# Kernel optimization log

Hardware: AMD Instinct MI355X
Metric: run time of the kernel (lower is better)

## Reference

```python
import jax, jax.numpy as jnp
import numpy as np

E = 8      # num_expert
D = 1024   # d_model
H = 2048   # expert hidden (htoh4 size)
K = 2      # top_k
N = 2048   # tokens (batch*seq)


def setup_inputs() -> dict:
    key = jax.random.key(0)
    ks = jax.random.split(key, 4)
    sc = lambda k, shape, s: jax.random.normal(k, shape, jnp.float32) * s
    return {
        "inp": jax.random.normal(ks[0], (N, D), jnp.float32),
        "Wg": sc(ks[1], (D, E), D ** -0.5),          # NaiveGate linear
        "bg": jnp.zeros((E,), jnp.float32),
        "W1": sc(ks[2], (E, D, H), D ** -0.5),        # per-expert htoh4
        "b1": jnp.zeros((E, H), jnp.float32),
        "W2": sc(ks[3], (E, H, D), H ** -0.5),        # per-expert h4toh
        "b2": jnp.zeros((E, D), jnp.float32),
    }


def reference(inp, Wg, bg, W1, b1, W2, b2):
    # NaiveGate: linear -> top_k logits -> softmax over the k selected logits
    logits = inp @ Wg + bg                              # [N, E]
    top_val, top_idx = jax.lax.top_k(logits, K)         # [N, K]
    gate_score = jax.nn.softmax(top_val, axis=-1)       # [N, K]

    # Expert grouped compute. Reference computes every expert on every token
    # (exact math, no capacity dropping); combine selects the routed ones.
    h = jax.nn.gelu(jnp.einsum('nd,edh->neh', inp, W1) + b1)   # [N, E, H]
    y = jnp.einsum('neh,ehd->ned', h, W2) + b2                 # [N, E, D]

    # Combine: equivalent to bmm(gate_score[N,1,K], x[N,K,D]) after gather.
    comb = jnp.sum(jax.nn.one_hot(top_idx, E, dtype=inp.dtype)
                   * gate_score[..., None], axis=1)            # [N, E]
    return jnp.einsum('ne,ned->nd', comb, y)                   # [N, D]
```

## Files before the change

kernel.cpp:

```cpp
#include <hip/hip_runtime.h>
#include <math.h>

#define N_TOK 2048
#define DM    1024
#define HD    2048
#define NE    8
#define RMAX  5120
#define TMAX  40

#define GATE_BLKS 512
#define XCVT_BLKS 1024
#define PREP_BLKS (GATE_BLKS + XCVT_BLKS)

typedef short short8 __attribute__((ext_vector_type(8)));
typedef unsigned short u16x8 __attribute__((ext_vector_type(8)));
typedef float f32x4  __attribute__((ext_vector_type(4)));

__device__ inline unsigned short f2b(float f) {
  unsigned int u = __float_as_uint(f);
  return (unsigned short)((u + 0x7FFFu + ((u >> 16) & 1u)) >> 16);
}
__device__ inline float b2f(unsigned short s) {
  return __uint_as_float(((unsigned int)s) << 16);
}
__device__ inline void gload_lds16(const void* g, void* l) {
  __builtin_amdgcn_global_load_lds(
      (const __attribute__((address_space(1))) unsigned int*)g,
      (__attribute__((address_space(3))) unsigned int*)l, 16, 0, 0);
}

__global__ __launch_bounds__(256) void prep_kernel(
    const float* __restrict__ inp, const float* __restrict__ Wg,
    const float* __restrict__ bg,
    int* __restrict__ top_idx, float* __restrict__ gate_w,
    unsigned short* __restrict__ Xb) {
  int bid = blockIdx.x;
  if (bid < GATE_BLKS) {
    int wave = threadIdx.x >> 6;
    int lane = threadIdx.x & 63;
    int n = bid * 4 + wave;
    float acc[NE];
#pragma unroll
    for (int e = 0; e < NE; ++e) acc[e] = 0.f;
    const float4* wg4 = reinterpret_cast<const float4*>(Wg);
#pragma unroll
    for (int i = 0; i < DM / 64; ++i) {
      int d = i * 64 + lane;
      float x = inp[n * DM + d];
      float4 w0 = wg4[d * 2 + 0];
      float4 w1 = wg4[d * 2 + 1];
      acc[0] += x * w0.x; acc[1] += x * w0.y; acc[2] += x * w0.z; acc[3] += x * w0.w;
      acc[4] += x * w1.x; acc[5] += x * w1.y; acc[6] += x * w1.z; acc[7] += x * w1.w;
    }
#pragma unroll
    for (int off = 32; off > 0; off >>= 1) {
#pragma unroll
      for (int e = 0; e < NE; ++e) acc[e] += __shfl_xor(acc[e], off);
    }
    if (lane == 0) {
      float v0 = -1e30f, v1 = -1e30f; int i0 = -1, i1 = -1;
#pragma unroll
      for (int e = 0; e < NE; ++e) {
        float v = acc[e] + bg[e];
        if (v > v0)      { v1 = v0; i1 = i0; v0 = v; i0 = e; }
        else if (v > v1) { v1 = v;  i1 = e; }
      }
      float e1 = expf(v1 - v0);
      float s  = 1.f + e1;
      top_idx[n * 2]     = i0;
      top_idx[n * 2 + 1] = i1;
      gate_w[n * 2]      = 1.f / s;
      gate_w[n * 2 + 1]  = e1 / s;
    }
  } else {
    int i = ((bid - GATE_BLKS) * 256 + threadIdx.x) * 8;
    float4 a = *(const float4*)(inp + i);
    float4 b = *(const float4*)(inp + i + 4);
    ushort4 pa, pb;
    pa.x = f2b(a.x); pa.y = f2b(a.y); pa.z = f2b(a.z); pa.w = f2b(a.w);
    pb.x = f2b(b.x); pb.y = f2b(b.y); pb.z = f2b(b.z); pb.w = f2b(b.w);
    *(ushort4*)(Xb + i)     = pa;
    *(ushort4*)(Xb + i + 4) = pb;
  }
}

__global__ __launch_bounds__(1024) void group_kernel(
    const int* __restrict__ top_idx,
    int* __restrict__ token_of, int* __restrict__ inv_g,
    int* __restrict__ tile_expert, int* __restrict__ tile_row0,
    int* __restrict__ n_tiles) {
  __shared__ int s_wtot[16];
  int tid = threadIdx.x, lane = tid & 63, wid = tid >> 6;
  int base = 0, tiles = 0;
  for (int e = 0; e < NE; ++e) {
    int cnt = 0;
#pragma unroll
    for (int c0 = 0; c0 < N_TOK; c0 += 1024) {
      int n = c0 + tid;
      int t0 = top_idx[n * 2], t1 = top_idx[n * 2 + 1];
      bool f = (t0 == e) || (t1 == e);
      int k = (t0 == e) ? 0 : 1;
      unsigned long long m = __ballot(f);
      int lp = __popcll(m & ((1ull << lane) - 1ull));
      if (lane == 0) s_wtot[wid] = __popcll(m);
      __syncthreads();
      int wbase = 0, tot = 0;
#pragma unroll
      for (int w = 0; w < 16; ++w) {
        int c = s_wtot[w];
        if (w < wid) wbase += c;
        tot += c;
      }
      if (f) {
        int pos = base + cnt + wbase + lp;
        token_of[pos] = n;
        inv_g[n * 2 + k] = pos;
      }
      cnt += tot;
      __syncthreads();
    }
    int padded = (cnt + 127) & ~127;
    for (int i = cnt + tid; i < padded; i += 1024) token_of[base + i] = -1;
    if (tid == 0) {
      for (int t = 0; t < padded / 128; ++t) {
        tile_expert[tiles + t] = e;
        tile_row0[tiles + t]   = base + t * 128;
      }
    }
    tiles += padded / 128;
    base  += padded;
    __syncthreads();
  }
  if (tid == 0) n_tiles[0] = tiles;
}

__global__ __launch_bounds__(256) void ffn1_mfma(
    const unsigned short* __restrict__ Xb,
    const float* __restrict__ W1,
    const float* __restrict__ b1,
    const unsigned short* __restrict__ zbuf,
    const int* __restrict__ token_of, const int* __restrict__ tile_expert,
    const int* __restrict__ tile_row0, const int* __restrict__ n_tiles,
    unsigned short* __restrict__ Hbuf) {
  if ((int)blockIdx.x >= n_tiles[0]) return;
  int e    = tile_expert[blockIdx.x];
  int row0 = tile_row0[blockIdx.x];
  int h0   = blockIdx.y * 64;
  __shared__ __align__(16) unsigned short Asl[128][32];
  __shared__ __align__(16) unsigned short Bsl[4][64][8];
  int tid = threadIdx.x, lane = tid & 63;
  int wid = tid >> 6, wr = wid >> 1, wc = wid & 1;
  int l15 = lane & 15, l4 = lane >> 4;
  int sw  = (l15 >> 1) & 3;

  int ar[2], asg[2], tk[2];
#pragma unroll
  for (int q = 0; q < 2; ++q) {
    int idx = tid + q * 256;
    ar[q]  = idx >> 2;
    asg[q] = (idx & 3) ^ ((ar[q] >> 1) & 3);
    tk[q]  = token_of[row0 + ar[q]];
  }
  int bcol = tid & 63, bks = tid >> 6;
  const float* bsrc = W1 + (size_t)e * DM * HD + (size_t)(bks * 8) * HD + h0 + bcol;

  f32x4 acc[4][2] = {};

  for (int kc = 0; kc < DM; kc += 32) {
    __syncthreads();
    float bv[8];
#pragma unroll
    for (int i = 0; i < 8; ++i) bv[i] = bsrc[(size_t)i * HD];
    bsrc += (size_t)32 * HD;
#pragma unroll
    for (int q = 0; q < 2; ++q) {
      int idx = tid + q * 256;
      const unsigned short* ga = (tk[q] < 0)
          ? zbuf
          : Xb + (size_t)tk[q] * DM + kc + asg[q] * 8;
      gload_lds16(ga, (char*)&Asl[0][0] + (size_t)idx * 16);
    }
    u16x8 bo;
#pragma unroll
    for (int i = 0; i < 8; ++i) bo[i] = f2b(bv[i]);
    *(u16x8*)&Bsl[bks][bcol][0] = bo;
    __syncthreads();
    short8 a[4], b[2];
#pragma unroll
    for (int m = 0; m < 4; ++m) {
      int R = wr * 64 + m * 16 + l15;
      a[m] = *(const short8*)((const char*)&Asl[0][0] + R * 64 + ((l4 ^ sw) << 4));
    }
#pragma unroll
    for (int n = 0; n < 2; ++n)
      b[n] = *(const short8*)&Bsl[l4][wc * 32 + n * 16 + l15][0];
#pragma unroll
    for (int m = 0; m < 4; ++m)
#pragma unroll
      for (int n = 0; n < 2; ++n)
        acc[m][n] = __builtin_amdgcn_mfma_f32_16x16x32_bf16(a[m], b[n], acc[m][n], 0, 0, 0);
  }

  float bias[2];
#pragma unroll
  for (int n = 0; n < 2; ++n) bias[n] = b1[e * HD + h0 + wc * 32 + n * 16 + l15];
#pragma unroll
  for (int m = 0; m < 4; ++m) {
#pragma unroll
    for (int n = 0; n < 2; ++n) {
      int col = h0 + wc * 32 + n * 16 + l15;
#pragma unroll
      for (int j = 0; j < 4; ++j) {
        int row = row0 + wr * 64 + m * 16 + l4 * 4 + j;
        float x = acc[m][n][j] + bias[n];
        float g = 0.5f * x * (1.f + tanhf(0.7978845608f * (x + 0.044715f * x * x * x)));
        Hbuf[(size_t)row * HD + col] = f2b(g);
      }
    }
  }
}

__global__ __launch_bounds__(256) void ffn2_mfma(
    const unsigned short* __restrict__ Hbuf,
    const float* __restrict__ W2,
    const float* __restrict__ b2,
    const int* __restrict__ tile_expert, const int* __restrict__ tile_row0,
    const int* __restrict__ n_tiles,
    unsigned short* __restrict__ Ybuf) {
  if ((int)blockIdx.x >= n_tiles[0]) return;
  int e    = tile_expert[blockIdx.x];
  int row0 = tile_row0[blockIdx.x];
  int d0   = blockIdx.y * 64;
  __shared__ __align__(16) unsigned short Asl[128][32];
  __shared__ __align__(16) unsigned short Bsl[4][64][8];
  int tid = threadIdx.x, lane = tid & 63;
  int wid = tid >> 6, wr = wid >> 1, wc = wid & 1;
  int l15 = lane & 15, l4 = lane >> 4;
  int sw  = (l15 >> 1) & 3;

  int ar[2], asg[2];
#pragma unroll
  for (int q = 0; q < 2; ++q) {
    int idx = tid + q * 256;
    ar[q]  = idx >> 2;
    asg[q] = (idx & 3) ^ ((ar[q] >> 1) & 3);
  }
  int bcol = tid & 63, bks = tid >> 6;
  const float* bsrc = W2 + (size_t)e * HD * DM + (size_t)(bks * 8) * DM + d0 + bcol;

  f32x4 acc[4][2] = {};

  for (int kc = 0; kc < HD; kc += 32) {
    __syncthreads();
    float bv[8];
#pragma unroll
    for (int i = 0; i < 8; ++i) bv[i] = bsrc[(size_t)i * DM];
    bsrc += (size_t)32 * DM;
#pragma unroll
    for (int q = 0; q < 2; ++q) {
      int idx = tid + q * 256;
      const unsigned short* ga =
          Hbuf + (size_t)(row0 + ar[q]) * HD + kc + asg[q] * 8;
      gload_lds16(ga, (char*)&Asl[0][0] + (size_t)idx * 16);
    }
    u16x8 bo;
#pragma unroll
    for (int i = 0; i < 8; ++i) bo[i] = f2b(bv[i]);
    *(u16x8*)&Bsl[bks][bcol][0] = bo;
    __syncthreads();
    short8 a[4], b[2];
#pragma unroll
    for (int m = 0; m < 4; ++m) {
      int R = wr * 64 + m * 16 + l15;
      a[m] = *(const short8*)((const char*)&Asl[0][0] + R * 64 + ((l4 ^ sw) << 4));
    }
#pragma unroll
    for (int n = 0; n < 2; ++n)
      b[n] = *(const short8*)&Bsl[l4][wc * 32 + n * 16 + l15][0];
#pragma unroll
    for (int m = 0; m < 4; ++m)
#pragma unroll
      for (int n = 0; n < 2; ++n)
        acc[m][n] = __builtin_amdgcn_mfma_f32_16x16x32_bf16(a[m], b[n], acc[m][n], 0, 0, 0);
  }

  float bias[2];
#pragma unroll
  for (int n = 0; n < 2; ++n) bias[n] = b2[e * DM + d0 + wc * 32 + n * 16 + l15];
#pragma unroll
  for (int m = 0; m < 4; ++m) {
#pragma unroll
    for (int n = 0; n < 2; ++n) {
      int col = d0 + wc * 32 + n * 16 + l15;
#pragma unroll
      for (int j = 0; j < 4; ++j) {
        int row = row0 + wr * 64 + m * 16 + l4 * 4 + j;
        Ybuf[(size_t)row * DM + col] = f2b(acc[m][n][j] + bias[n]);
      }
    }
  }
}

__global__ void combine_kernel(const unsigned short* __restrict__ Ybuf,
                               const int* __restrict__ inv_g,
                               const float* __restrict__ gate_w,
                               float* __restrict__ out) {
  int n = blockIdx.x;
  int r0 = inv_g[n * 2], r1 = inv_g[n * 2 + 1];
  float g0 = gate_w[n * 2], g1 = gate_w[n * 2 + 1];
  int i = threadIdx.x;
  ushort4 a = *(const ushort4*)(Ybuf + (size_t)r0 * DM + i * 4);
  ushort4 b = *(const ushort4*)(Ybuf + (size_t)r1 * DM + i * 4);
  float4 rv;
  rv.x = g0 * b2f(a.x) + g1 * b2f(b.x);
  rv.y = g0 * b2f(a.y) + g1 * b2f(b.y);
  rv.z = g0 * b2f(a.z) + g1 * b2f(b.z);
  rv.w = g0 * b2f(a.w) + g1 * b2f(b.w);
  *(float4*)(out + (size_t)n * DM + i * 4) = rv;
}

extern "C" void kernel_launch(void* const* d_in, const int* in_sizes, int n_in,
                              void* d_out, int out_size, void* d_ws, size_t ws_size,
                              hipStream_t stream) {
  const float* inp = (const float*)d_in[0];
  const float* Wg  = (const float*)d_in[1];
  const float* bg  = (const float*)d_in[2];
  const float* W1  = (const float*)d_in[3];
  const float* b1  = (const float*)d_in[4];
  const float* W2  = (const float*)d_in[5];
  const float* b2  = (const float*)d_in[6];
  float* out = (float*)d_out;

  char* ws = (char*)d_ws;
  size_t off = 0;
  auto alloc = [&](size_t bytes) {
    size_t o = off;
    off = (off + bytes + 255) & ~(size_t)255;
    return o;
  };
  int*   top_idx     = (int*)  (ws + alloc(N_TOK * 2 * sizeof(int)));
  float* gate_w      = (float*)(ws + alloc(N_TOK * 2 * sizeof(float)));
  int*   token_of    = (int*)  (ws + alloc(RMAX * sizeof(int)));
  int*   inv_g       = (int*)  (ws + alloc(N_TOK * 2 * sizeof(int)));
  int*   tile_expert = (int*)  (ws + alloc(TMAX * sizeof(int)));
  int*   tile_row0   = (int*)  (ws + alloc(TMAX * sizeof(int)));
  int*   n_tiles     = (int*)  (ws + alloc(sizeof(int)));
  unsigned short* zbuf = (unsigned short*)(ws + alloc(256));
  unsigned short* Xb   = (unsigned short*)(ws + alloc((size_t)N_TOK * DM * 2));
  unsigned short* Hbuf = (unsigned short*)(ws + alloc((size_t)RMAX * HD * 2));
  unsigned short* Ybuf = (unsigned short*)(ws + alloc((size_t)RMAX * DM * 2));
  (void)ws_size;

  hipMemsetAsync(zbuf, 0, 256, stream);
  prep_kernel<<<PREP_BLKS, 256, 0, stream>>>(inp, Wg, bg, top_idx, gate_w, Xb);
  group_kernel<<<1, 1024, 0, stream>>>(top_idx, token_of, inv_g,
                                       tile_expert, tile_row0, n_tiles);
  ffn1_mfma<<<dim3(TMAX, HD / 64), 256, 0, stream>>>(
      Xb, W1, b1, zbuf, token_of, tile_expert, tile_row0, n_tiles, Hbuf);
  ffn2_mfma<<<dim3(TMAX, DM / 64), 256, 0, stream>>>(
      Hbuf, W2, b2, tile_expert, tile_row0, n_tiles, Ybuf);
  combine_kernel<<<N_TOK, 256, 0, stream>>>(Ybuf, inv_g, gate_w, out);
}
```

Measured before the change: 168.0 us.

## Keep per-expert weight slice resident in LDS and loop over row tiles

FFN kernels now launch one block per (expert, output column slice). Each block converts its whole fp32 weight slice to bf16 once into LDS (128 KB), then loops over all 128-row tiles of that expert. A operands are read straight from global memory without LDS staging. This removes the repeated fp32 weight loads and bf16 conversions that previously happened once per row tile. In exchange the grids shrink to 256 blocks, and per-block work scales with expert load, which risks imbalance and low occupancy.

```diff
diff --git a/kernel.cpp b/kernel.cpp
--- a/kernel.cpp
+++ b/kernel.cpp
@@ -6,7 +6,6 @@
 #define HD    2048
 #define NE    8
 #define RMAX  5120
-#define TMAX  40
 
 #define GATE_BLKS 512
 #define XCVT_BLKS 1024
@@ -22,11 +21,6 @@
 }
 __device__ inline float b2f(unsigned short s) {
   return __uint_as_float(((unsigned int)s) << 16);
-}
-__device__ inline void gload_lds16(const void* g, void* l) {
-  __builtin_amdgcn_global_load_lds(
-      (const __attribute__((address_space(1))) unsigned int*)g,
-      (__attribute__((address_space(3))) unsigned int*)l, 16, 0, 0);
 }
 
 __global__ __launch_bounds__(256) void prep_kernel(
@@ -87,11 +81,10 @@
 __global__ __launch_bounds__(1024) void group_kernel(
     const int* __restrict__ top_idx,
     int* __restrict__ token_of, int* __restrict__ inv_g,
-    int* __restrict__ tile_expert, int* __restrict__ tile_row0,
-    int* __restrict__ n_tiles) {
+    int* __restrict__ exp_base, int* __restrict__ exp_nt) {
   __shared__ int s_wtot[16];
   int tid = threadIdx.x, lane = tid & 63, wid = tid >> 6;
-  int base = 0, tiles = 0;
+  int base = 0;
   for (int e = 0; e < NE; ++e) {
     int cnt = 0;
 #pragma unroll
@@ -121,181 +114,144 @@
     }
     int padded = (cnt + 127) & ~127;
     for (int i = cnt + tid; i < padded; i += 1024) token_of[base + i] = -1;
-    if (tid == 0) {
-      for (int t = 0; t < padded / 128; ++t) {
-        tile_expert[tiles + t] = e;
-        tile_row0[tiles + t]   = base + t * 128;
-      }
-    }
-    tiles += padded / 128;
-    base  += padded;
+    if (tid == 0) { exp_base[e] = base; exp_nt[e] = padded / 128; }
+    base += padded;
     __syncthreads();
   }
-  if (tid == 0) n_tiles[0] = tiles;
-}
-
-__global__ __launch_bounds__(256) void ffn1_mfma(
+}
+
+__global__ __launch_bounds__(512, 2) void ffn1_mfma(
     const unsigned short* __restrict__ Xb,
     const float* __restrict__ W1,
     const float* __restrict__ b1,
-    const unsigned short* __restrict__ zbuf,
-    const int* __restrict__ token_of, const int* __restrict__ tile_expert,
-    const int* __restrict__ tile_row0, const int* __restrict__ n_tiles,
+    const unsigned short* __restrict__ Xzero,
+    const int* __restrict__ token_of,
+    const int* __restrict__ exp_base, const int* __restrict__ exp_nt,
     unsigned short* __restrict__ Hbuf) {
-  if ((int)blockIdx.x >= n_tiles[0]) return;
-  int e    = tile_expert[blockIdx.x];
-  int row0 = tile_row0[blockIdx.x];
-  int h0   = blockIdx.y * 64;
-  __shared__ __align__(16) unsigned short Asl[128][32];
-  __shared__ __align__(16) unsigned short Bsl[4][64][8];
+  int e  = blockIdx.x;
+  int h0 = blockIdx.y * 64;
+  __shared__ __align__(16) unsigned short Wl[128][64][8];
   int tid = threadIdx.x, lane = tid & 63;
   int wid = tid >> 6, wr = wid >> 1, wc = wid & 1;
   int l15 = lane & 15, l4 = lane >> 4;
-  int sw  = (l15 >> 1) & 3;
-
-  int ar[2], asg[2], tk[2];
-#pragma unroll
-  for (int q = 0; q < 2; ++q) {
-    int idx = tid + q * 256;
-    ar[q]  = idx >> 2;
-    asg[q] = (idx & 3) ^ ((ar[q] >> 1) & 3);
-    tk[q]  = token_of[row0 + ar[q]];
-  }
-  int bcol = tid & 63, bks = tid >> 6;
-  const float* bsrc = W1 + (size_t)e * DM * HD + (size_t)(bks * 8) * HD + h0 + bcol;
-
-  f32x4 acc[4][2] = {};
-
-  for (int kc = 0; kc < DM; kc += 32) {
-    __syncthreads();
-    float bv[8];
-#pragma unroll
-    for (int i = 0; i < 8; ++i) bv[i] = bsrc[(size_t)i * HD];
-    bsrc += (size_t)32 * HD;
-#pragma unroll
-    for (int q = 0; q < 2; ++q) {
-      int idx = tid + q * 256;
-      const unsigned short* ga = (tk[q] < 0)
-          ? zbuf
-          : Xb + (size_t)tk[q] * DM + kc + asg[q] * 8;
-      gload_lds16(ga, (char*)&Asl[0][0] + (size_t)idx * 16);
-    }
-    u16x8 bo;
-#pragma unroll
-    for (int i = 0; i < 8; ++i) bo[i] = f2b(bv[i]);
-    *(u16x8*)&Bsl[bks][bcol][0] = bo;
-    __syncthreads();
-    short8 a[4], b[2];
-#pragma unroll
-    for (int m = 0; m < 4; ++m) {
-      int R = wr * 64 + m * 16 + l15;
-      a[m] = *(const short8*)((const char*)&Asl[0][0] + R * 64 + ((l4 ^ sw) << 4));
-    }
-#pragma unroll
-    for (int n = 0; n < 2; ++n)
-      b[n] = *(const short8*)&Bsl[l4][wc * 32 + n * 16 + l15][0];
-#pragma unroll
-    for (int m = 0; m < 4; ++m)
-#pragma unroll
-      for (int n = 0; n < 2; ++n)
-        acc[m][n] = __builtin_amdgcn_mfma_f32_16x16x32_bf16(a[m], b[n], acc[m][n], 0, 0, 0);
-  }
+
+  {
+    const float* W1e = W1 + (size_t)e * DM * HD + h0;
+    int scol = tid & 63, skg = tid >> 6;
+#pragma unroll
+    for (int kko = 0; kko < 16; ++kko) {
+      int kb = kko * 8 + skg;
+      const float* s = W1e + (size_t)(kb * 8) * HD + scol;
+      float v[8];
+#pragma unroll
+      for (int i = 0; i < 8; ++i) v[i] = s[(size_t)i * HD];
+      u16x8 o;
+#pragma unroll
+      for (int i = 0; i < 8; ++i) o[i] = f2b(v[i]);
+      *(u16x8*)&Wl[kb][scol][0] = o;
+    }
+  }
+  __syncthreads();
 
   float bias[2];
 #pragma unroll
   for (int n = 0; n < 2; ++n) bias[n] = b1[e * HD + h0 + wc * 32 + n * 16 + l15];
-#pragma unroll
-  for (int m = 0; m < 4; ++m) {
-#pragma unroll
-    for (int n = 0; n < 2; ++n) {
-      int col = h0 + wc * 32 + n * 16 + l15;
-#pragma unroll
-      for (int j = 0; j < 4; ++j) {
-        int row = row0 + wr * 64 + m * 16 + l4 * 4 + j;
-        float x = acc[m][n][j] + bias[n];
-        float g = 0.5f * x * (1.f + tanhf(0.7978845608f * (x + 0.044715f * x * x * x)));
-        Hbuf[(size_t)row * HD + col] = f2b(g);
-      }
-    }
-  }
-}
-
-__global__ __launch_bounds__(256) void ffn2_mfma(
+
+  int nt = exp_nt[e];
+  int base0 = exp_base[e];
+  for (int rt = 0; rt < nt; ++rt) {
+    int row0 = base0 + rt * 128;
+    const unsigned short* abase0;
+    const unsigned short* abase1;
+    {
+      int tk0 = token_of[row0 + wr * 32 + l15];
+      int tk1 = token_of[row0 + wr * 32 + 16 + l15];
+      abase0 = (tk0 < 0) ? Xzero : Xb + (size_t)tk0 * DM;
+      abase1 = (tk1 < 0) ? Xzero : Xb + (size_t)tk1 * DM;
+    }
+    f32x4 acc[2][2] = {};
+    for (int ks = 0; ks < 32; ++ks) {
+      short8 a0 = *(const short8*)(abase0 + ks * 32 + l4 * 8);
+      short8 a1 = *(const short8*)(abase1 + ks * 32 + l4 * 8);
+      short8 b0 = *(const short8*)&Wl[ks * 4 + l4][wc * 32 + l15][0];
+      short8 b1v = *(const short8*)&Wl[ks * 4 + l4][wc * 32 + 16 + l15][0];
+      acc[0][0] = __builtin_amdgcn_mfma_f32_16x16x32_bf16(a0, b0,  acc[0][0], 0, 0, 0);
+      acc[0][1] = __builtin_amdgcn_mfma_f32_16x16x32_bf16(a0, b1v, acc[0][1], 0, 0, 0);
+      acc[1][0] = __builtin_amdgcn_mfma_f32_16x16x32_bf16(a1, b0,  acc[1][0], 0, 0, 0);
+      acc[1][1] = __builtin_amdgcn_mfma_f32_16x16x32_bf16(a1, b1v, acc[1][1], 0, 0, 0);
+    }
+#pragma unroll
+    for (int m = 0; m < 2; ++m) {
+#pragma unroll
+      for (int n = 0; n < 2; ++n) {
+        int col = h0 + wc * 32 + n * 16 + l15;
+#pragma unroll
+        for (int j = 0; j < 4; ++j) {
+          int row = row0 + wr * 32 + m * 16 + l4 * 4 + j;
+          float x = acc[m][n][j] + bias[n];
+          float g = 0.5f * x * (1.f + tanhf(0.7978845608f * (x + 0.044715f * x * x * x)));
+          Hbuf[(size_t)row * HD + col] = f2b(g);
+        }
+      }
+    }
+  }
+}
+
+__global__ __launch_bounds__(512, 2) void ffn2_mfma(
     const unsigned short* __restrict__ Hbuf,
     const float* __restrict__ W2,
     const float* __restrict__ b2,
-    const int* __restrict__ tile_expert, const int* __restrict__ tile_row0,
-    const int* __restrict__ n_tiles,
+    const int* __restrict__ exp_base, const int* __restrict__ exp_nt,
     unsigned short* __restrict__ Ybuf) {
-  if ((int)blockIdx.x >= n_tiles[0]) return;
-  int e    = tile_expert[blockIdx.x];
-  int row0 = tile_row0[blockIdx.x];
-  int d0   = blockIdx.y * 64;
-  __shared__ __align__(16) unsigned short Asl[128][32];
-  __shared__ __align__(16) unsigned short Bsl[4][64][8];
+  int e  = blockIdx.x;
+  int d0 = blockIdx.y * 32;
+  __shared__ __align__(16) unsigned short Wl[256][32][8];
   int tid = threadIdx.x, lane = tid & 63;
-  int wid = tid >> 6, wr = wid >> 1, wc = wid & 1;
+  int wr = tid >> 6;
   int l15 = lane & 15, l4 = lane >> 4;
-  int sw  = (l15 >> 1) & 3;
-
-  int ar[2], asg[2];
-#pragma unroll
-  for (int q = 0; q < 2; ++q) {
-    int idx = tid + q * 256;
-    ar[q]  = idx >> 2;
-    asg[q] = (idx & 3) ^ ((ar[q] >> 1) & 3);
-  }
-  int bcol = tid & 63, bks = tid >> 6;
-  const float* bsrc = W2 + (size_t)e * HD * DM + (size_t)(bks * 8) * DM + d0 + bcol;
-
-  f32x4 acc[4][2] = {};
-
-  for (int kc = 0; kc < HD; kc += 32) {
-    __syncthreads();
-    float bv[8];
-#pragma unroll
-    for (int i = 0; i < 8; ++i) bv[i] = bsrc[(size_t)i * DM];
-    bsrc += (size_t)32 * DM;
-#pragma unroll
-    for (int q = 0; q < 2; ++q) {
-      int idx = tid + q * 256;
-      const unsigned short* ga =
-          Hbuf + (size_t)(row0 + ar[q]) * HD + kc + asg[q] * 8;
-      gload_lds16(ga, (char*)&Asl[0][0] + (size_t)idx * 16);
-    }
-    u16x8 bo;
-#pragma unroll
-    for (int i = 0; i < 8; ++i) bo[i] = f2b(bv[i]);
-    *(u16x8*)&Bsl[bks][bcol][0] = bo;
-    __syncthreads();
-    short8 a[4], b[2];
-#pragma unroll
-    for (int m = 0; m < 4; ++m) {
-      int R = wr * 64 + m * 16 + l15;
-      a[m] = *(const short8*)((const char*)&Asl[0][0] + R * 64 + ((l4 ^ sw) << 4));
-    }
-#pragma unroll
-    for (int n = 0; n < 2; ++n)
-      b[n] = *(const short8*)&Bsl[l4][wc * 32 + n * 16 + l15][0];
-#pragma unroll
-    for (int m = 0; m < 4; ++m)
-#pragma unroll
-      for (int n = 0; n < 2; ++n)
-        acc[m][n] = __builtin_amdgcn_mfma_f32_16x16x32_bf16(a[m], b[n], acc[m][n], 0, 0, 0);
-  }
+
+  {
+    const float* W2e = W2 + (size_t)e * HD * DM + d0;
+    int scol = tid & 31, skg = tid >> 5;
+#pragma unroll
+    for (int kko = 0; kko < 16; ++kko) {
+      int kb = kko * 16 + skg;
+      const float* s = W2e + (size_t)(kb * 8) * DM + scol;
+      float v[8];
+#pragma unroll
+      for (int i = 0; i < 8; ++i) v[i] = s[(size_t)i * DM];
+      u16x8 o;
+#pragma unroll
+      for (int i = 0; i < 8; ++i) o[i] = f2b(v[i]);
+      *(u16x8*)&Wl[kb][scol][0] = o;
+    }
+  }
+  __syncthreads();
 
   float bias[2];
 #pragma unroll
-  for (int n = 0; n < 2; ++n) bias[n] = b2[e * DM + d0 + wc * 32 + n * 16 + l15];
-#pragma unroll
-  for (int m = 0; m < 4; ++m) {
+  for (int n = 0; n < 2; ++n) bias[n] = b2[e * DM + d0 + n * 16 + l15];
+
+  int nt = exp_nt[e];
+  int base0 = exp_base[e];
+  for (int rt = 0; rt < nt; ++rt) {
+    int row0 = base0 + rt * 128;
+    const unsigned short* abase = Hbuf + (size_t)(row0 + wr * 16 + l15) * HD;
+    f32x4 acc[2] = {};
+    for (int ks = 0; ks < 64; ++ks) {
+      short8 a  = *(const short8*)(abase + ks * 32 + l4 * 8);
+      short8 b0 = *(const short8*)&Wl[ks * 4 + l4][l15][0];
+      short8 b1v = *(const short8*)&Wl[ks * 4 + l4][16 + l15][0];
+      acc[0] = __builtin_amdgcn_mfma_f32_16x16x32_bf16(a, b0,  acc[0], 0, 0, 0);
+      acc[1] = __builtin_amdgcn_mfma_f32_16x16x32_bf16(a, b1v, acc[1], 0, 0, 0);
+    }
 #pragma unroll
     for (int n = 0; n < 2; ++n) {
-      int col = d0 + wc * 32 + n * 16 + l15;
+      int col = d0 + n * 16 + l15;
 #pragma unroll
       for (int j = 0; j < 4; ++j) {
-        int row = row0 + wr * 64 + m * 16 + l4 * 4 + j;
-        Ybuf[(size_t)row * DM + col] = f2b(acc[m][n][j] + bias[n]);
+        int row = row0 + wr * 16 + l4 * 4 + j;
+        Ybuf[(size_t)row * DM + col] = f2b(acc[n][j] + bias[n]);
       }
     }
   }
@@ -338,26 +294,24 @@
     off = (off + bytes + 255) & ~(size_t)255;
     return o;
   };
-  int*   top_idx     = (int*)  (ws + alloc(N_TOK * 2 * sizeof(int)));
-  float* gate_w      = (float*)(ws + alloc(N_TOK * 2 * sizeof(float)));
-  int*   token_of    = (int*)  (ws + alloc(RMAX * sizeof(int)));
-  int*   inv_g       = (int*)  (ws + alloc(N_TOK * 2 * sizeof(int)));
-  int*   tile_expert = (int*)  (ws + alloc(TMAX * sizeof(int)));
-  int*   tile_row0   = (int*)  (ws + alloc(TMAX * sizeof(int)));
-  int*   n_tiles     = (int*)  (ws + alloc(sizeof(int)));
-  unsigned short* zbuf = (unsigned short*)(ws + alloc(256));
-  unsigned short* Xb   = (unsigned short*)(ws + alloc((size_t)N_TOK * DM * 2));
-  unsigned short* Hbuf = (unsigned short*)(ws + alloc((size_t)RMAX * HD * 2));
-  unsigned short* Ybuf = (unsigned short*)(ws + alloc((size_t)RMAX * DM * 2));
+  int*   top_idx  = (int*)  (ws + alloc(N_TOK * 2 * sizeof(int)));
+  float* gate_w   = (float*)(ws + alloc(N_TOK * 2 * sizeof(float)));
+  int*   token_of = (int*)  (ws + alloc(RMAX * sizeof(int)));
+  int*   inv_g    = (int*)  (ws + alloc(N_TOK * 2 * sizeof(int)));
+  int*   exp_base = (int*)  (ws + alloc(NE * sizeof(int)));
+  int*   exp_nt   = (int*)  (ws + alloc(NE * sizeof(int)));
+  unsigned short* Xzero = (unsigned short*)(ws + alloc(DM * 2));
+  unsigned short* Xb    = (unsigned short*)(ws + alloc((size_t)N_TOK * DM * 2));
+  unsigned short* Hbuf  = (unsigned short*)(ws + alloc((size_t)RMAX * HD * 2));
+  unsigned short* Ybuf  = (unsigned short*)(ws + alloc((size_t)RMAX * DM * 2));
   (void)ws_size;
 
-  hipMemsetAsync(zbuf, 0, 256, stream);
+  hipMemsetAsync(Xzero, 0, DM * 2, stream);
   prep_kernel<<<PREP_BLKS, 256, 0, stream>>>(inp, Wg, bg, top_idx, gate_w, Xb);
-  group_kernel<<<1, 1024, 0, stream>>>(top_idx, token_of, inv_g,
-                                       tile_expert, tile_row0, n_tiles);
-  ffn1_mfma<<<dim3(TMAX, HD / 64), 256, 0, stream>>>(
-      Xb, W1, b1, zbuf, token_of, tile_expert, tile_row0, n_tiles, Hbuf);
-  ffn2_mfma<<<dim3(TMAX, DM / 64), 256, 0, stream>>>(
-      Hbuf, W2, b2, tile_expert, tile_row0, n_tiles, Ybuf);
+  group_kernel<<<1, 1024, 0, stream>>>(top_idx, token_of, inv_g, exp_base, exp_nt);
+  ffn1_mfma<<<dim3(NE, HD / 64), 512, 0, stream>>>(
+      Xb, W1, b1, Xzero, token_of, exp_base, exp_nt, Hbuf);
+  ffn2_mfma<<<dim3(NE, DM / 32), 512, 0, stream>>>(
+      Hbuf, W2, b2, exp_base, exp_nt, Ybuf);
   combine_kernel<<<N_TOK, 256, 0, stream>>>(Ybuf, inv_g, gate_w, out);
 }
```

Result: slower. 359.4 us (+114.0%).

## Double-buffer LDS tiles in expert FFN GEMMs to overlap loads with MFMA

Applied to the files above, without the earlier changes.

Both expert GEMM kernels now keep two LDS buffers for the A and B tiles. The global loads for the next k-step are issued before the MFMAs of the current step, which removes one barrier per iteration and hides load latency behind compute. Launch bounds now request 4 blocks per CU, which caps register use. The cost is twice the LDS footprint, extra register pressure from holding two B prefetch arrays, and a larger zero buffer for padded rows.

```diff
diff --git a/kernel.cpp b/kernel.cpp
--- a/kernel.cpp
+++ b/kernel.cpp
@@ -134,11 +134,11 @@
   if (tid == 0) n_tiles[0] = tiles;
 }
 
-__global__ __launch_bounds__(256) void ffn1_mfma(
+__global__ __launch_bounds__(256, 4) void ffn1_mfma(
     const unsigned short* __restrict__ Xb,
     const float* __restrict__ W1,
     const float* __restrict__ b1,
-    const unsigned short* __restrict__ zbuf,
+    const unsigned short* __restrict__ Xzero,
     const int* __restrict__ token_of, const int* __restrict__ tile_expert,
     const int* __restrict__ tile_row0, const int* __restrict__ n_tiles,
     unsigned short* __restrict__ Hbuf) {
@@ -146,8 +146,8 @@
   int e    = tile_expert[blockIdx.x];
   int row0 = tile_row0[blockIdx.x];
   int h0   = blockIdx.y * 64;
-  __shared__ __align__(16) unsigned short Asl[128][32];
-  __shared__ __align__(16) unsigned short Bsl[4][64][8];
+  __shared__ __align__(16) unsigned short Asl[2][128][32];
+  __shared__ __align__(16) unsigned short Bsl[2][4][64][8];
   int tid = threadIdx.x, lane = tid & 63;
   int wid = tid >> 6, wr = wid >> 1, wc = wid & 1;
   int l15 = lane & 15, l4 = lane >> 4;
@@ -162,43 +162,60 @@
     tk[q]  = token_of[row0 + ar[q]];
   }
   int bcol = tid & 63, bks = tid >> 6;
-  const float* bsrc = W1 + (size_t)e * DM * HD + (size_t)(bks * 8) * HD + h0 + bcol;
+  const float* W1e = W1 + (size_t)e * DM * HD;
 
   f32x4 acc[4][2] = {};
-
-  for (int kc = 0; kc < DM; kc += 32) {
-    __syncthreads();
-    float bv[8];
-#pragma unroll
-    for (int i = 0; i < 8; ++i) bv[i] = bsrc[(size_t)i * HD];
-    bsrc += (size_t)32 * HD;
+  float bvA[8], bvB[8];
+
+  auto issueB = [&](int t, float* bv) {
+    const float* p = W1e + (size_t)(t * 32 + bks * 8) * HD + h0 + bcol;
+#pragma unroll
+    for (int i = 0; i < 8; ++i) bv[i] = p[(size_t)i * HD];
+  };
+  auto packwrite = [&](const float* bv, int buf) {
+    u16x8 o;
+#pragma unroll
+    for (int i = 0; i < 8; ++i) o[i] = f2b(bv[i]);
+    *(u16x8*)&Bsl[buf][bks][bcol][0] = o;
+  };
+  auto issueA = [&](int t, int buf) {
 #pragma unroll
     for (int q = 0; q < 2; ++q) {
       int idx = tid + q * 256;
       const unsigned short* ga = (tk[q] < 0)
-          ? zbuf
-          : Xb + (size_t)tk[q] * DM + kc + asg[q] * 8;
-      gload_lds16(ga, (char*)&Asl[0][0] + (size_t)idx * 16);
-    }
-    u16x8 bo;
-#pragma unroll
-    for (int i = 0; i < 8; ++i) bo[i] = f2b(bv[i]);
-    *(u16x8*)&Bsl[bks][bcol][0] = bo;
-    __syncthreads();
+          ? Xzero
+          : Xb + (size_t)tk[q] * DM + t * 32 + asg[q] * 8;
+      gload_lds16(ga, (char*)&Asl[buf][0][0] + (size_t)idx * 16);
+    }
+  };
+  auto compute = [&](int buf) {
     short8 a[4], b[2];
 #pragma unroll
     for (int m = 0; m < 4; ++m) {
       int R = wr * 64 + m * 16 + l15;
-      a[m] = *(const short8*)((const char*)&Asl[0][0] + R * 64 + ((l4 ^ sw) << 4));
+      a[m] = *(const short8*)((const char*)&Asl[buf][0][0] + R * 64 + ((l4 ^ sw) << 4));
     }
 #pragma unroll
     for (int n = 0; n < 2; ++n)
-      b[n] = *(const short8*)&Bsl[l4][wc * 32 + n * 16 + l15][0];
+      b[n] = *(const short8*)&Bsl[buf][l4][wc * 32 + n * 16 + l15][0];
 #pragma unroll
     for (int m = 0; m < 4; ++m)
 #pragma unroll
       for (int n = 0; n < 2; ++n)
         acc[m][n] = __builtin_amdgcn_mfma_f32_16x16x32_bf16(a[m], b[n], acc[m][n], 0, 0, 0);
+  };
+
+  issueB(0, bvA);
+  issueA(0, 0);
+  for (int t = 0; t < 32; t += 2) {
+    packwrite(bvA, 0);
+    __syncthreads();
+    if (t + 1 < 32) { issueB(t + 1, bvB); issueA(t + 1, 1); }
+    compute(0);
+    packwrite(bvB, 1);
+    __syncthreads();
+    if (t + 2 < 32) { issueB(t + 2, bvA); issueA(t + 2, 0); }
+    compute(1);
   }
 
   float bias[2];
@@ -220,7 +237,7 @@
   }
 }
 
-__global__ __launch_bounds__(256) void ffn2_mfma(
+__global__ __launch_bounds__(256, 4) void ffn2_mfma(
     const unsigned short* __restrict__ Hbuf,
     const float* __restrict__ W2,
     const float* __restrict__ b2,
@@ -231,8 +248,8 @@
   int e    = tile_expert[blockIdx.x];
   int row0 = tile_row0[blockIdx.x];
   int d0   = blockIdx.y * 64;
-  __shared__ __align__(16) unsigned short Asl[128][32];
-  __shared__ __align__(16) unsigned short Bsl[4][64][8];
+  __shared__ __align__(16) unsigned short Asl[2][128][32];
+  __shared__ __align__(16) unsigned short Bsl[2][4][64][8];
   int tid = threadIdx.x, lane = tid & 63;
   int wid = tid >> 6, wr = wid >> 1, wc = wid & 1;
   int l15 = lane & 15, l4 = lane >> 4;
@@ -246,42 +263,59 @@
     asg[q] = (idx & 3) ^ ((ar[q] >> 1) & 3);
   }
   int bcol = tid & 63, bks = tid >> 6;
-  const float* bsrc = W2 + (size_t)e * HD * DM + (size_t)(bks * 8) * DM + d0 + bcol;
+  const float* W2e = W2 + (size_t)e * HD * DM;
 
   f32x4 acc[4][2] = {};
-
-  for (int kc = 0; kc < HD; kc += 32) {
-    __syncthreads();
-    float bv[8];
-#pragma unroll
-    for (int i = 0; i < 8; ++i) bv[i] = bsrc[(size_t)i * DM];
-    bsrc += (size_t)32 * DM;
+  float bvA[8], bvB[8];
+
+  auto issueB = [&](int t, float* bv) {
+    const float* p = W2e + (size_t)(t * 32 + bks * 8) * DM + d0 + bcol;
+#pragma unroll
+    for (int i = 0; i < 8; ++i) bv[i] = p[(size_t)i * DM];
+  };
+  auto packwrite = [&](const float* bv, int buf) {
+    u16x8 o;
+#pragma unroll
+    for (int i = 0; i < 8; ++i) o[i] = f2b(bv[i]);
+    *(u16x8*)&Bsl[buf][bks][bcol][0] = o;
+  };
+  auto issueA = [&](int t, int buf) {
 #pragma unroll
     for (int q = 0; q < 2; ++q) {
       int idx = tid + q * 256;
       const unsigned short* ga =
-          Hbuf + (size_t)(row0 + ar[q]) * HD + kc + asg[q] * 8;
-      gload_lds16(ga, (char*)&Asl[0][0] + (size_t)idx * 16);
-    }
-    u16x8 bo;
-#pragma unroll
-    for (int i = 0; i < 8; ++i) bo[i] = f2b(bv[i]);
-    *(u16x8*)&Bsl[bks][bcol][0] = bo;
-    __syncthreads();
+          Hbuf + (size_t)(row0 + ar[q]) * HD + t * 32 + asg[q] * 8;
+      gload_lds16(ga, (char*)&Asl[buf][0][0] + (size_t)idx * 16);
+    }
+  };
+  auto compute = [&](int buf) {
     short8 a[4], b[2];
 #pragma unroll
     for (int m = 0; m < 4; ++m) {
       int R = wr * 64 + m * 16 + l15;
-      a[m] = *(const short8*)((const char*)&Asl[0][0] + R * 64 + ((l4 ^ sw) << 4));
+      a[m] = *(const short8*)((const char*)&Asl[buf][0][0] + R * 64 + ((l4 ^ sw) << 4));
     }
 #pragma unroll
     for (int n = 0; n < 2; ++n)
-      b[n] = *(const short8*)&Bsl[l4][wc * 32 + n * 16 + l15][0];
+      b[n] = *(const short8*)&Bsl[buf][l4][wc * 32 + n * 16 + l15][0];
 #pragma unroll
     for (int m = 0; m < 4; ++m)
 #pragma unroll
       for (int n = 0; n < 2; ++n)
         acc[m][n] = __builtin_amdgcn_mfma_f32_16x16x32_bf16(a[m], b[n], acc[m][n], 0, 0, 0);
+  };
+
+  issueB(0, bvA);
+  issueA(0, 0);
+  for (int t = 0; t < 64; t += 2) {
+    packwrite(bvA, 0);
+    __syncthreads();
+    if (t + 1 < 64) { issueB(t + 1, bvB); issueA(t + 1, 1); }
+    compute(0);
+    packwrite(bvB, 1);
+    __syncthreads();
+    if (t + 2 < 64) { issueB(t + 2, bvA); issueA(t + 2, 0); }
+    compute(1);
   }
 
   float bias[2];
@@ -345,18 +379,18 @@
   int*   tile_expert = (int*)  (ws + alloc(TMAX * sizeof(int)));
   int*   tile_row0   = (int*)  (ws + alloc(TMAX * sizeof(int)));
   int*   n_tiles     = (int*)  (ws + alloc(sizeof(int)));
-  unsigned short* zbuf = (unsigned short*)(ws + alloc(256));
-  unsigned short* Xb   = (unsigned short*)(ws + alloc((size_t)N_TOK * DM * 2));
-  unsigned short* Hbuf = (unsigned short*)(ws + alloc((size_t)RMAX * HD * 2));
-  unsigned short* Ybuf = (unsigned short*)(ws + alloc((size_t)RMAX * DM * 2));
+  unsigned short* Xzero = (unsigned short*)(ws + alloc(DM * 2));
+  unsigned short* Xb    = (unsigned short*)(ws + alloc((size_t)N_TOK * DM * 2));
+  unsigned short* Hbuf  = (unsigned short*)(ws + alloc((size_t)RMAX * HD * 2));
+  unsigned short* Ybuf  = (unsigned short*)(ws + alloc((size_t)RMAX * DM * 2));
   (void)ws_size;
 
-  hipMemsetAsync(zbuf, 0, 256, stream);
+  hipMemsetAsync(Xzero, 0, DM * 2, stream);
   prep_kernel<<<PREP_BLKS, 256, 0, stream>>>(inp, Wg, bg, top_idx, gate_w, Xb);
   group_kernel<<<1, 1024, 0, stream>>>(top_idx, token_of, inv_g,
                                        tile_expert, tile_row0, n_tiles);
   ffn1_mfma<<<dim3(TMAX, HD / 64), 256, 0, stream>>>(
-      Xb, W1, b1, zbuf, token_of, tile_expert, tile_row0, n_tiles, Hbuf);
+      Xb, W1, b1, Xzero, token_of, tile_expert, tile_row0, n_tiles, Hbuf);
   ffn2_mfma<<<dim3(TMAX, DM / 64), 256, 0, stream>>>(
       Hbuf, W2, b2, tile_expert, tile_row0, n_tiles, Ybuf);
   combine_kernel<<<N_TOK, 256, 0, stream>>>(Ybuf, inv_g, gate_w, out);
```

After: 175.7 us. 4.6% more time.
